# Performance work log

Measured on AMD Instinct MI355X. Metric: run time of the kernel, lower is better.

Reference implementation:

```python
import jax, jax.numpy as jnp
import numpy as np

DIM, CDIM, CSIZE = 512, 128, 8192
EPS = 1e-6


def setup_inputs() -> dict:
    key = jax.random.key(0)
    k = jax.random.split(key, 5)
    x = jax.random.normal(k[0], (4, 4096, DIM), jnp.float32)
    codebook = jax.random.normal(k[1], (CSIZE, CDIM), jnp.float32) * CDIM ** -0.5
    W1 = jax.random.normal(k[2], (CDIM, DIM), jnp.float32) * CDIM ** -0.5
    b1 = jnp.zeros((DIM,), jnp.float32)
    W2 = jax.random.normal(k[3], (DIM, DIM), jnp.float32) * DIM ** -0.5
    b2 = jnp.zeros((DIM,), jnp.float32)
    return dict(x=x, codebook=codebook, W1=W1, b1=b1, W2=W2, b2=b2)


def _code_transform(cb, W1, b1, W2, b2):
    # linear then residual(SELU -> linear):  h + Linear(SELU(h))
    h = cb @ W1 + b1                      # [C, dim]
    return h + jax.nn.selu(h) @ W2 + b2


def _rotate_to(src, tgt):
    # Householder-based rotation trick; only src (=x) carries gradient.
    ns = jnp.linalg.norm(src, axis=-1, keepdims=True)
    nt = jnp.linalg.norm(tgt, axis=-1, keepdims=True)
    u = jax.lax.stop_gradient(src / jnp.maximum(ns, EPS))
    q = jax.lax.stop_gradient(tgt / jnp.maximum(nt, EPS))
    w = u + q
    w = jax.lax.stop_gradient(w / jnp.maximum(jnp.linalg.norm(w, axis=-1, keepdims=True), EPS))
    rot = (src
           - 2.0 * jnp.sum(src * w, -1, keepdims=True) * w
           + 2.0 * jnp.sum(src * u, -1, keepdims=True) * q)
    return rot * jax.lax.stop_gradient(nt / jnp.maximum(ns, EPS))


def reference(x, codebook, W1, b1, W2, b2):
    # implicit codebook through learned transform  [C, dim]
    icb = _code_transform(codebook, W1, b1, W2, b2)
    # nearest-code search (no_grad in original): squared euclidean, argmin
    x_sg = jax.lax.stop_gradient(x)
    icb_sg = jax.lax.stop_gradient(icb)
    d2 = (jnp.sum(x_sg * x_sg, -1, keepdims=True)
          - 2.0 * jnp.einsum('bnd,cd->bnc', x_sg, icb_sg)
          + jnp.sum(icb_sg * icb_sg, -1))          # [B,N,C]
    indices = jnp.argmin(d2, axis=-1)               # [B,N]
    quantized = icb[indices]                        # [B,N,dim]
    commit_loss = (jnp.mean((jax.lax.stop_gradient(x) - quantized) ** 2)
                   + 0.25 * jnp.mean((x - jax.lax.stop_gradient(quantized)) ** 2))
    quantized = _rotate_to(x, quantized)
    return quantized, indices, commit_loss
```

## Files before the change

kernel.cpp:

```cpp
#include <hip/hip_runtime.h>
#include <math.h>

#define DIM   512
#define CDIM  128
#define CSIZE 8192
#define NTOK  16384
#define EPSV  1e-6f
#define NSLICE 8

#define SELU_SCALE 1.0507009873554805f
#define SELU_ALPHA 1.6732632423543772f

typedef __bf16 bf16x8 __attribute__((ext_vector_type(8)));
typedef float  f32x4  __attribute__((ext_vector_type(4)));
typedef unsigned short u16x8 __attribute__((ext_vector_type(8)));

__device__ __forceinline__ float selu_f(float v) {
    return SELU_SCALE * (v > 0.f ? v : SELU_ALPHA * expm1f(v));
}

__device__ __forceinline__ unsigned short b16(float f) {
    unsigned u = __float_as_uint(f);
    u += 0x7FFFu + ((u >> 16) & 1u);
    return (unsigned short)(u >> 16);
}
__device__ __forceinline__ float b2f(unsigned short h) {
    return __uint_as_float(((unsigned)h) << 16);
}

__device__ __forceinline__ unsigned SWZ(unsigned b) {
    return b ^ (((b >> 6) & 14u) << 3);
}

#define GLOAD16(g, l) __builtin_amdgcn_global_load_lds( \
    (const __attribute__((address_space(1))) void*)(g),  \
    (__attribute__((address_space(3))) void*)(l), 16, 0, 0)

__global__ __launch_bounds__(256) void k_init(float* __restrict__ rn2,
                                              float* __restrict__ lossacc) {
    const int i = blockIdx.x * 256 + threadIdx.x;
    if (i < CSIZE) rn2[i] = 0.f;
    if (i < 64)    lossacc[i] = 0.f;
}

__global__ void k_fin(const float* __restrict__ lossacc, float* __restrict__ out_loss) {
    float v = lossacc[threadIdx.x];
#pragma unroll
    for (int o = 1; o < 64; o <<= 1) v += __shfl_xor(v, o);
    if (threadIdx.x == 0)
        out_loss[0] = 1.25f * v / (float)((size_t)NTOK * DIM);
}

__global__ __launch_bounds__(256) void k_split(const float* __restrict__ in,
                                               unsigned short* __restrict__ hi,
                                               unsigned short* __restrict__ lo,
                                               int n4) {
    const int i = blockIdx.x * 256 + threadIdx.x;
    if (i >= n4) return;
    const float4 v = ((const float4*)in)[i];
    const unsigned short h0 = b16(v.x), h1 = b16(v.y), h2 = b16(v.z), h3 = b16(v.w);
    const unsigned short l0 = b16(v.x - b2f(h0));
    const unsigned short l1 = b16(v.y - b2f(h1));
    const unsigned short l2 = b16(v.z - b2f(h2));
    const unsigned short l3 = b16(v.w - b2f(h3));
    ((ushort4*)hi)[i] = make_ushort4(h0, h1, h2, h3);
    ((ushort4*)lo)[i] = make_ushort4(l0, l1, l2, l3);
}

__global__ __launch_bounds__(256) void k_splitT(const float* __restrict__ W,
                                                unsigned short* __restrict__ Thi,
                                                unsigned short* __restrict__ Tlo,
                                                int K, int N) {
    __shared__ float t[32][33];
    const int tx = threadIdx.x & 31, ty = threadIdx.x >> 5;
    const int n0 = blockIdx.x * 32, k0 = blockIdx.y * 32;
#pragma unroll
    for (int i = 0; i < 4; ++i)
        t[ty + i * 8][tx] = W[(size_t)(k0 + ty + i * 8) * N + n0 + tx];
    __syncthreads();
#pragma unroll
    for (int i = 0; i < 4; ++i) {
        const int n = n0 + ty + i * 8, k = k0 + tx;
        const float v = t[tx][ty + i * 8];
        const unsigned short h = b16(v);
        Thi[(size_t)n * K + k] = h;
        Tlo[(size_t)n * K + k] = b16(v - b2f(h));
    }
}

template<int KTOT, bool OUT_SPLIT>
__global__ __launch_bounds__(256) void k_gemm(const float* __restrict__ A,
                                              const unsigned short* __restrict__ BThi,
                                              const unsigned short* __restrict__ BTlo,
                                              const float* __restrict__ bias,
                                              const float* __restrict__ res,
                                              float* __restrict__ outF,
                                              unsigned short* __restrict__ outHi,
                                              unsigned short* __restrict__ outLo,
                                              float* __restrict__ rn2) {
    __shared__ __align__(16) unsigned char smem[24576];
    const int tid = threadIdx.x;
    const int wave = tid >> 6, lane = tid & 63;
    const int l15 = lane & 15, l4 = lane >> 4;
    const int m0 = blockIdx.x * 128, n0 = blockIdx.y * 64;
    const int wm0 = (wave >> 1) * 64, wn0 = (wave & 1) * 32;

    const unsigned LB = SWZ((unsigned)tid * 16u);
    const int soffB = (int)(LB >> 6) * KTOT + (int)((LB >> 4) & 3) * 8;

    const unsigned ra0 = SWZ((unsigned)((wm0 + l15) * 64 + l4 * 16));
    const unsigned rb0 = SWZ((unsigned)((wn0 + l15) * 64 + l4 * 16));

    f32x4 acc[4][2];
#pragma unroll
    for (int a = 0; a < 4; ++a)
#pragma unroll
        for (int b = 0; b < 2; ++b) acc[a][b] = (f32x4)(0.f);

    for (int k0 = 0; k0 < KTOT; k0 += 32) {
        __syncthreads();
        GLOAD16(BThi + (size_t)n0 * KTOT + k0 + soffB, smem + 16384 + wave * 1024);
        GLOAD16(BTlo + (size_t)n0 * KTOT + k0 + soffB, smem + 20480 + wave * 1024);
#pragma unroll
        for (int r = 0; r < 2; ++r) {
            const unsigned g = (unsigned)(tid + r * 256) * 16u;
            const int grow = (int)(g >> 6), gel = (int)((g >> 4) & 3) * 8;
            const float4 v0 = *(const float4*)(A + (size_t)(m0 + grow) * KTOT + k0 + gel);
            const float4 v1 = *(const float4*)(A + (size_t)(m0 + grow) * KTOT + k0 + gel + 4);
            float s[8] = {v0.x, v0.y, v0.z, v0.w, v1.x, v1.y, v1.z, v1.w};
            u16x8 hv, lv;
#pragma unroll
            for (int j = 0; j < 8; ++j) {
                const float sv = OUT_SPLIT ? selu_f(s[j]) : s[j];
                const unsigned short hb = b16(sv);
                hv[j] = hb;
                lv[j] = b16(sv - b2f(hb));
            }
            const unsigned d = SWZ(g);
            *(u16x8*)(smem + d) = hv;
            *(u16x8*)(smem + 8192 + d) = lv;
        }
        __syncthreads();

        bf16x8 bh[2], bl[2];
#pragma unroll
        for (int ni = 0; ni < 2; ++ni) {
            bh[ni] = *(const bf16x8*)(smem + 16384 + rb0 + ni * 1024);
            bl[ni] = *(const bf16x8*)(smem + 20480 + rb0 + ni * 1024);
        }
#pragma unroll
        for (int mi = 0; mi < 4; ++mi) {
            const bf16x8 ah = *(const bf16x8*)(smem + ra0 + mi * 1024);
            const bf16x8 al = *(const bf16x8*)(smem + 8192 + ra0 + mi * 1024);
#pragma unroll
            for (int ni = 0; ni < 2; ++ni) {
                acc[mi][ni] = __builtin_amdgcn_mfma_f32_16x16x32_bf16(ah, bh[ni], acc[mi][ni], 0, 0, 0);
                acc[mi][ni] = __builtin_amdgcn_mfma_f32_16x16x32_bf16(ah, bl[ni], acc[mi][ni], 0, 0, 0);
                acc[mi][ni] = __builtin_amdgcn_mfma_f32_16x16x32_bf16(al, bh[ni], acc[mi][ni], 0, 0, 0);
            }
        }
    }
#pragma unroll
    for (int mi = 0; mi < 4; ++mi)
#pragma unroll
        for (int rr = 0; rr < 4; ++rr) {
            const int m = m0 + wm0 + mi * 16 + l4 * 4 + rr;
            float s2 = 0.f;
#pragma unroll
            for (int ni = 0; ni < 2; ++ni) {
                const int n = n0 + wn0 + ni * 16 + l15;
                float v = acc[mi][ni][rr] + bias[n];
                if constexpr (OUT_SPLIT) {
                    v += res[(size_t)m * DIM + n];
                    const unsigned short hb = b16(v);
                    outHi[(size_t)m * DIM + n] = hb;
                    outLo[(size_t)m * DIM + n] = b16(v - b2f(hb));
                    s2 = fmaf(v, v, s2);
                } else {
                    outF[(size_t)m * DIM + n] = v;
                }
            }
            if constexpr (OUT_SPLIT) {
#pragma unroll
                for (int o = 1; o < 16; o <<= 1) s2 += __shfl_xor(s2, o);
                if (l15 == 0) atomicAdd(&rn2[m], s2);
            }
        }
}

__global__ __launch_bounds__(512, 2) void k_dist(const unsigned short* __restrict__ xh,
                                                 const unsigned short* __restrict__ xl,
                                                 const unsigned short* __restrict__ ch,
                                                 const unsigned short* __restrict__ cl,
                                                 const float* __restrict__ rn2,
                                                 float* __restrict__ pval,
                                                 int*   __restrict__ pidx) {
    __shared__ __align__(16) unsigned char smem[131072];
    const int tid  = threadIdx.x;
    const int wave = tid >> 6, lane = tid & 63;
    const int l15 = lane & 15, l4 = lane >> 4;
    const int m0   = blockIdx.x * 256;
    const int wm0  = (wave >> 1) * 64;
    const int wn0  = (wave & 1) * 128;

    const unsigned LS = SWZ((unsigned)tid * 16u);
    const int soff0 = (int)(LS >> 6) * DIM + (int)((LS >> 4) & 3) * 8;

    const unsigned ra0 = SWZ((unsigned)((wm0 + l15) * 64 + l4 * 16));
    const unsigned rb0 = SWZ((unsigned)((wn0 + l15) * 64 + l4 * 16));

    const unsigned short* xhb = xh + (size_t)m0 * DIM;
    const unsigned short* xlb = xl + (size_t)m0 * DIM;
    const int cbase = blockIdx.y * (CSIZE / NSLICE);

    constexpr int NT   = (CSIZE / NSLICE) / 256;
    constexpr int TOTI = NT * (DIM / 32);

    auto stage = [&](int iter, unsigned bufbase) {
        const int nt2 = iter >> 4;
        const int k0n = (iter & 15) * 32;
        const int sA  = soff0 + k0n;
        const size_t cb0 = (size_t)(cbase + nt2 * 256) * DIM;
#pragma unroll
        for (int r = 0; r < 2; ++r) {
            GLOAD16(xhb + sA + r * 128 * DIM,      smem + bufbase + 0     + r * 8192 + wave * 1024);
            GLOAD16(xlb + sA + r * 128 * DIM,      smem + bufbase + 16384 + r * 8192 + wave * 1024);
            GLOAD16(ch + cb0 + sA + r * 128 * DIM, smem + bufbase + 32768 + r * 8192 + wave * 1024);
            GLOAD16(cl + cb0 + sA + r * 128 * DIM, smem + bufbase + 49152 + r * 8192 + wave * 1024);
        }
    };

    float bestv[4][4];
    int   besti[4][4];
#pragma unroll
    for (int a = 0; a < 4; ++a)
#pragma unroll
        for (int b = 0; b < 4; ++b) { bestv[a][b] = 3.0e38f; besti[a][b] = 0; }

    stage(0, 0u);
    __syncthreads();
    unsigned cur = 0;

    for (int nt = 0; nt < NT; ++nt) {
        f32x4 acc[4][8];
#pragma unroll
        for (int a = 0; a < 4; ++a)
#pragma unroll
            for (int b = 0; b < 8; ++b) acc[a][b] = (f32x4)(0.f);

        for (int ks = 0; ks < 16; ++ks) {
            const int iter = nt * 16 + ks;
            if (iter + 1 < TOTI) stage(iter + 1, (cur ^ 1u) * 65536u);

            const unsigned char* base = smem + cur * 65536u;
            bf16x8 ah[4], al[4];
#pragma unroll
            for (int mi = 0; mi < 4; ++mi) {
                ah[mi] = *(const bf16x8*)(base + ra0 + mi * 1024);
                al[mi] = *(const bf16x8*)(base + 16384 + ra0 + mi * 1024);
            }
#pragma unroll
            for (int ni = 0; ni < 8; ++ni) {
                const bf16x8 bh = *(const bf16x8*)(base + 32768 + rb0 + ni * 1024);
                const bf16x8 bl = *(const bf16x8*)(base + 49152 + rb0 + ni * 1024);
#pragma unroll
                for (int mi = 0; mi < 4; ++mi) {
                    acc[mi][ni] = __builtin_amdgcn_mfma_f32_16x16x32_bf16(ah[mi], bh, acc[mi][ni], 0, 0, 0);
                    acc[mi][ni] = __builtin_amdgcn_mfma_f32_16x16x32_bf16(ah[mi], bl, acc[mi][ni], 0, 0, 0);
                    acc[mi][ni] = __builtin_amdgcn_mfma_f32_16x16x32_bf16(al[mi], bh, acc[mi][ni], 0, 0, 0);
                }
            }
            __syncthreads();
            cur ^= 1u;
        }

        const int n0 = cbase + nt * 256;
#pragma unroll
        for (int ni = 0; ni < 8; ++ni) {
            const int n = n0 + wn0 + ni * 16 + l15;
            const float r = rn2[n];
#pragma unroll
            for (int mi = 0; mi < 4; ++mi)
#pragma unroll
                for (int rr = 0; rr < 4; ++rr) {
                    const float v = fmaf(-2.f, acc[mi][ni][rr], r);
                    if (v < bestv[mi][rr]) { bestv[mi][rr] = v; besti[mi][rr] = n; }
                }
        }
    }

    __syncthreads();
    float* vbuf = (float*)smem;
    int*   ibuf = (int*)(smem + 2048);
#pragma unroll
    for (int mi = 0; mi < 4; ++mi)
#pragma unroll
        for (int rr = 0; rr < 4; ++rr) {
            float v = bestv[mi][rr];
            int   id = besti[mi][rr];
#pragma unroll
            for (int o = 1; o < 16; o <<= 1) {
                const float ov = __shfl_xor(v, o);
                const int   oid = __shfl_xor(id, o);
                if (ov < v || (ov == v && oid < id)) { v = ov; id = oid; }
            }
            if (l15 == 0) {
                const int ml = wm0 + mi * 16 + l4 * 4 + rr;
                vbuf[(wave & 1) * 256 + ml] = v;
                ibuf[(wave & 1) * 256 + ml] = id;
            }
        }
    __syncthreads();
    if (tid < 256) {
        const int ml = tid;
        float v0 = vbuf[ml], v1 = vbuf[256 + ml];
        int   i0 = ibuf[ml], i1 = ibuf[256 + ml];
        if (v1 < v0 || (v1 == v0 && i1 < i0)) { v0 = v1; i0 = i1; }
        pval[(size_t)blockIdx.y * NTOK + m0 + ml] = v0;
        pidx[(size_t)blockIdx.y * NTOK + m0 + ml] = i0;
    }
}

__global__ __launch_bounds__(256) void k_epi(const float* __restrict__ x,
                                             const unsigned short* __restrict__ chi,
                                             const unsigned short* __restrict__ clo,
                                             const float* __restrict__ pval,
                                             const int*   __restrict__ pidx,
                                             float* __restrict__ out_q,
                                             float* __restrict__ out_idx,
                                             float* __restrict__ lossacc) {
    const int wave = threadIdx.x >> 6, lane = threadIdx.x & 63;
    const int t = blockIdx.x * 4 + wave;

    float v = 3.0e38f; int id = 0;
    if (lane < NSLICE) {
        v  = pval[(size_t)lane * NTOK + t];
        id = pidx[(size_t)lane * NTOK + t];
    }
#pragma unroll
    for (int o = 1; o < 16; o <<= 1) {
        const float ov = __shfl_xor(v, o);
        const int   oid = __shfl_xor(id, o);
        if (ov < v || (ov == v && oid < id)) { v = ov; id = oid; }
    }
    id = __shfl(id, 0);

    const float4* xp = (const float4*)(x + (size_t)t * DIM);
    const float4 xv0 = xp[lane * 2];
    const float4 xv1 = xp[lane * 2 + 1];
    const u16x8 hv = *(const u16x8*)(chi + (size_t)id * DIM + lane * 8);
    const u16x8 lv = *(const u16x8*)(clo + (size_t)id * DIM + lane * 8);
    float q[8], xs[8] = {xv0.x, xv0.y, xv0.z, xv0.w, xv1.x, xv1.y, xv1.z, xv1.w};
#pragma unroll
    for (int j = 0; j < 8; ++j) q[j] = b2f(hv[j]) + b2f(lv[j]);

    float p0 = 0.f, p1 = 0.f, p2 = 0.f;
#pragma unroll
    for (int j = 0; j < 8; ++j) {
        p0 = fmaf(xs[j], xs[j], p0);
        p1 = fmaf(q[j], q[j], p1);
        p2 = fmaf(xs[j], q[j], p2);
    }
#pragma unroll
    for (int o = 1; o < 64; o <<= 1) {
        p0 += __shfl_xor(p0, o);
        p1 += __shfl_xor(p1, o);
        p2 += __shfl_xor(p2, o);
    }
    const float sx2 = p0, sq2 = p1, sxq = p2;

    const float ns  = sqrtf(sx2);
    const float nt  = sqrtf(sq2);
    const float nsc = fmaxf(ns, EPSV);
    const float ntc = fmaxf(nt, EPSV);
    const float xu  = sx2 / nsc;
    const float xqh = sxq / ntc;
    const float xw0 = xu + xqh;
    const float w0n2 = sx2 / (nsc * nsc) + 2.f * sxq / (nsc * ntc) + sq2 / (ntc * ntc);
    const float w0nc = fmaxf(sqrtf(w0n2), EPSV);
    const float coefW = 2.f * xw0 / (w0nc * w0nc);
    const float coefQ = 2.f * xu / ntc;
    const float scale = nt / nsc;
    const float cx = scale * (1.f - coefW / nsc);
    const float cq = scale * (coefQ - coefW / ntc);

    float4 ov0, ov1;
    ov0.x = cx * xs[0] + cq * q[0];  ov0.y = cx * xs[1] + cq * q[1];
    ov0.z = cx * xs[2] + cq * q[2];  ov0.w = cx * xs[3] + cq * q[3];
    ov1.x = cx * xs[4] + cq * q[4];  ov1.y = cx * xs[5] + cq * q[5];
    ov1.z = cx * xs[6] + cq * q[6];  ov1.w = cx * xs[7] + cq * q[7];
    ((float4*)(out_q + (size_t)t * DIM))[lane * 2]     = ov0;
    ((float4*)(out_q + (size_t)t * DIM))[lane * 2 + 1] = ov1;

    __shared__ float sew[4];
    if (lane == 0) {
        out_idx[t] = (float)id;
        sew[wave] = sx2 - 2.f * sxq + sq2;
    }
    __syncthreads();
    if (threadIdx.x == 0) {
        const float se = sew[0] + sew[1] + sew[2] + sew[3];
        atomicAdd(lossacc + (blockIdx.x & 63), se);
    }
}

extern "C" void kernel_launch(void* const* d_in, const int* in_sizes, int n_in,
                              void* d_out, int out_size, void* d_ws, size_t ws_size,
                              hipStream_t stream) {
    const float* x  = (const float*)d_in[0];
    const float* cb = (const float*)d_in[1];
    const float* W1 = (const float*)d_in[2];
    const float* b1 = (const float*)d_in[3];
    const float* W2 = (const float*)d_in[4];
    const float* b2 = (const float*)d_in[5];

    char* ws = (char*)d_ws;
    float* h = (float*)ws;
    unsigned short* chi = (unsigned short*)(h + (size_t)CSIZE * DIM);
    unsigned short* clo = chi + (size_t)CSIZE * DIM;
    unsigned short* W1Thi = clo + (size_t)CSIZE * DIM;
    unsigned short* W1Tlo = W1Thi + (size_t)DIM * CDIM;
    unsigned short* W2Thi = W1Tlo + (size_t)DIM * CDIM;
    unsigned short* W2Tlo = W2Thi + (size_t)DIM * DIM;
    float* rn2  = (float*)(W2Tlo + (size_t)DIM * DIM);
    float* pval = rn2 + CSIZE;
    int*   pidx = (int*)(pval + (size_t)NSLICE * NTOK);
    float* lossacc = (float*)(pidx + (size_t)NSLICE * NTOK);

    unsigned short* xhi = (unsigned short*)d_out;
    unsigned short* xlo = xhi + (size_t)NTOK * DIM;

    float* out_q    = (float*)d_out;
    float* out_idx  = out_q + (size_t)NTOK * DIM;
    float* out_loss = out_idx + NTOK;

    k_init<<<(CSIZE + 255) / 256, 256, 0, stream>>>(rn2, lossacc);
    k_split<<<(NTOK * DIM / 4) / 256, 256, 0, stream>>>(x, xhi, xlo, NTOK * DIM / 4);
    k_splitT<<<dim3(DIM / 32, CDIM / 32), 256, 0, stream>>>(W1, W1Thi, W1Tlo, CDIM, DIM);
    k_splitT<<<dim3(DIM / 32, DIM / 32), 256, 0, stream>>>(W2, W2Thi, W2Tlo, DIM, DIM);
    k_gemm<CDIM, false><<<dim3(CSIZE / 128, DIM / 64), 256, 0, stream>>>(
        cb, W1Thi, W1Tlo, b1, nullptr, h, nullptr, nullptr, nullptr);
    k_gemm<DIM, true><<<dim3(CSIZE / 128, DIM / 64), 256, 0, stream>>>(
        h, W2Thi, W2Tlo, b2, h, nullptr, chi, clo, rn2);
    k_dist<<<dim3(NTOK / 256, NSLICE), 512, 0, stream>>>(xhi, xlo, chi, clo, rn2, pval, pidx);
    k_epi<<<NTOK / 4, 256, 0, stream>>>(x, chi, clo, pval, pidx, out_q, out_idx, lossacc);
    k_fin<<<1, 64, 0, stream>>>(lossacc, out_loss);
}
```

Measured before the change: 485.5 us.

## Load distance-kernel A operands directly into registers and shrink blocks to 128 tokens

The distance kernel now stages only the codebook tile in shared memory. The token hi/lo fragments are loaded straight from global memory into double-buffered registers, and blocks shrink to 256 threads and 128 tokens with half the LDS. The in-block cross-wave argmin reduction through shared memory is dropped. Each wave writes its own partial result, so the epilogue now reduces 16 slices instead of 8. MFMA sections get raised wave priority. This removes LDS traffic and barriers for A, at the cost of uncoalesced per-lane global loads for A and doubled codebook re-reads across blocks.

```diff
diff --git a/kernel.cpp b/kernel.cpp
--- a/kernel.cpp
+++ b/kernel.cpp
@@ -7,6 +7,7 @@
 #define NTOK  16384
 #define EPSV  1e-6f
 #define NSLICE 8
+#define NSLICE2 16
 
 #define SELU_SCALE 1.0507009873554805f
 #define SELU_ALPHA 1.6732632423543772f
@@ -188,45 +189,49 @@
         }
 }
 
-__global__ __launch_bounds__(512, 2) void k_dist(const unsigned short* __restrict__ xh,
+__global__ __launch_bounds__(256, 2) void k_dist(const unsigned short* __restrict__ xh,
                                                  const unsigned short* __restrict__ xl,
                                                  const unsigned short* __restrict__ ch,
                                                  const unsigned short* __restrict__ cl,
                                                  const float* __restrict__ rn2,
                                                  float* __restrict__ pval,
                                                  int*   __restrict__ pidx) {
-    __shared__ __align__(16) unsigned char smem[131072];
+    __shared__ __align__(16) unsigned char smem[65536];
     const int tid  = threadIdx.x;
     const int wave = tid >> 6, lane = tid & 63;
     const int l15 = lane & 15, l4 = lane >> 4;
-    const int m0   = blockIdx.x * 256;
+    const int m0   = blockIdx.x * 128;
     const int wm0  = (wave >> 1) * 64;
     const int wn0  = (wave & 1) * 128;
 
     const unsigned LS = SWZ((unsigned)tid * 16u);
     const int soff0 = (int)(LS >> 6) * DIM + (int)((LS >> 4) & 3) * 8;
 
-    const unsigned ra0 = SWZ((unsigned)((wm0 + l15) * 64 + l4 * 16));
     const unsigned rb0 = SWZ((unsigned)((wn0 + l15) * 64 + l4 * 16));
 
-    const unsigned short* xhb = xh + (size_t)m0 * DIM;
-    const unsigned short* xlb = xl + (size_t)m0 * DIM;
+    const unsigned short* xhb = xh + (size_t)(m0 + wm0 + l15) * DIM + l4 * 8;
+    const unsigned short* xlb = xl + (size_t)(m0 + wm0 + l15) * DIM + l4 * 8;
+
     const int cbase = blockIdx.y * (CSIZE / NSLICE);
-
     constexpr int NT   = (CSIZE / NSLICE) / 256;
-    constexpr int TOTI = NT * (DIM / 32);
-
-    auto stage = [&](int iter, unsigned bufbase) {
-        const int nt2 = iter >> 4;
-        const int k0n = (iter & 15) * 32;
-        const int sA  = soff0 + k0n;
-        const size_t cb0 = (size_t)(cbase + nt2 * 256) * DIM;
-#pragma unroll
-        for (int r = 0; r < 2; ++r) {
-            GLOAD16(xhb + sA + r * 128 * DIM,      smem + bufbase + 0     + r * 8192 + wave * 1024);
-            GLOAD16(xlb + sA + r * 128 * DIM,      smem + bufbase + 16384 + r * 8192 + wave * 1024);
-            GLOAD16(ch + cb0 + sA + r * 128 * DIM, smem + bufbase + 32768 + r * 8192 + wave * 1024);
-            GLOAD16(cl + cb0 + sA + r * 128 * DIM, smem + bufbase + 49152 + r * 8192 + wave * 1024);
+    constexpr int TOTI = NT * 16;
+
+    auto stageB = [&](int it, unsigned bufbase) {
+        const size_t cb0 = (size_t)(cbase + (it >> 4) * 256) * DIM + (it & 15) * 32 + soff0;
+#pragma unroll
+        for (int r = 0; r < 4; ++r) {
+            GLOAD16(ch + cb0 + r * 64 * DIM, smem + bufbase + 0     + r * 4096 + wave * 1024);
+            GLOAD16(cl + cb0 + r * 64 * DIM, smem + bufbase + 16384 + r * 4096 + wave * 1024);
+        }
+    };
+
+    bf16x8 aH[2][4], aL[2][4];
+    auto loadA = [&](int it, int par) {
+        const int k0 = (it & 15) * 32;
+#pragma unroll
+        for (int f = 0; f < 4; ++f) {
+            aH[par][f] = *(const bf16x8*)(xhb + (size_t)f * 16 * DIM + k0);
+            aL[par][f] = *(const bf16x8*)(xlb + (size_t)f * 16 * DIM + k0);
         }
     };
 
@@ -237,7 +242,8 @@
 #pragma unroll
         for (int b = 0; b < 4; ++b) { bestv[a][b] = 3.0e38f; besti[a][b] = 0; }
 
-    stage(0, 0u);
+    stageB(0, 0u);
+    loadA(0, 0);
     __syncthreads();
     unsigned cur = 0;
 
@@ -248,28 +254,27 @@
 #pragma unroll
             for (int b = 0; b < 8; ++b) acc[a][b] = (f32x4)(0.f);
 
+#pragma unroll
         for (int ks = 0; ks < 16; ++ks) {
-            const int iter = nt * 16 + ks;
-            if (iter + 1 < TOTI) stage(iter + 1, (cur ^ 1u) * 65536u);
-
-            const unsigned char* base = smem + cur * 65536u;
-            bf16x8 ah[4], al[4];
-#pragma unroll
-            for (int mi = 0; mi < 4; ++mi) {
-                ah[mi] = *(const bf16x8*)(base + ra0 + mi * 1024);
-                al[mi] = *(const bf16x8*)(base + 16384 + ra0 + mi * 1024);
-            }
+            const int it = nt * 16 + ks;
+            if (it + 1 < TOTI) {
+                stageB(it + 1, (cur ^ 1u) * 32768u);
+                loadA(it + 1, (ks + 1) & 1);
+            }
+            const unsigned char* base = smem + cur * 32768u;
+            __builtin_amdgcn_s_setprio(1);
 #pragma unroll
             for (int ni = 0; ni < 8; ++ni) {
-                const bf16x8 bh = *(const bf16x8*)(base + 32768 + rb0 + ni * 1024);
-                const bf16x8 bl = *(const bf16x8*)(base + 49152 + rb0 + ni * 1024);
+                const bf16x8 bh = *(const bf16x8*)(base + rb0 + ni * 1024);
+                const bf16x8 bl = *(const bf16x8*)(base + 16384 + rb0 + ni * 1024);
 #pragma unroll
                 for (int mi = 0; mi < 4; ++mi) {
-                    acc[mi][ni] = __builtin_amdgcn_mfma_f32_16x16x32_bf16(ah[mi], bh, acc[mi][ni], 0, 0, 0);
-                    acc[mi][ni] = __builtin_amdgcn_mfma_f32_16x16x32_bf16(ah[mi], bl, acc[mi][ni], 0, 0, 0);
-                    acc[mi][ni] = __builtin_amdgcn_mfma_f32_16x16x32_bf16(al[mi], bh, acc[mi][ni], 0, 0, 0);
+                    acc[mi][ni] = __builtin_amdgcn_mfma_f32_16x16x32_bf16(aH[ks & 1][mi], bh, acc[mi][ni], 0, 0, 0);
+                    acc[mi][ni] = __builtin_amdgcn_mfma_f32_16x16x32_bf16(aH[ks & 1][mi], bl, acc[mi][ni], 0, 0, 0);
+                    acc[mi][ni] = __builtin_amdgcn_mfma_f32_16x16x32_bf16(aL[ks & 1][mi], bh, acc[mi][ni], 0, 0, 0);
                 }
             }
+            __builtin_amdgcn_s_setprio(0);
             __syncthreads();
             cur ^= 1u;
         }
@@ -289,9 +294,7 @@
         }
     }
 
-    __syncthreads();
-    float* vbuf = (float*)smem;
-    int*   ibuf = (int*)(smem + 2048);
+    const int slice = blockIdx.y * 2 + (wave & 1);
 #pragma unroll
     for (int mi = 0; mi < 4; ++mi)
 #pragma unroll
@@ -305,20 +308,11 @@
                 if (ov < v || (ov == v && oid < id)) { v = ov; id = oid; }
             }
             if (l15 == 0) {
-                const int ml = wm0 + mi * 16 + l4 * 4 + rr;
-                vbuf[(wave & 1) * 256 + ml] = v;
-                ibuf[(wave & 1) * 256 + ml] = id;
-            }
-        }
-    __syncthreads();
-    if (tid < 256) {
-        const int ml = tid;
-        float v0 = vbuf[ml], v1 = vbuf[256 + ml];
-        int   i0 = ibuf[ml], i1 = ibuf[256 + ml];
-        if (v1 < v0 || (v1 == v0 && i1 < i0)) { v0 = v1; i0 = i1; }
-        pval[(size_t)blockIdx.y * NTOK + m0 + ml] = v0;
-        pidx[(size_t)blockIdx.y * NTOK + m0 + ml] = i0;
-    }
+                const int m = m0 + wm0 + mi * 16 + l4 * 4 + rr;
+                pval[(size_t)slice * NTOK + m] = v;
+                pidx[(size_t)slice * NTOK + m] = id;
+            }
+        }
 }
 
 __global__ __launch_bounds__(256) void k_epi(const float* __restrict__ x,
@@ -333,7 +327,7 @@
     const int t = blockIdx.x * 4 + wave;
 
     float v = 3.0e38f; int id = 0;
-    if (lane < NSLICE) {
+    if (lane < NSLICE2) {
         v  = pval[(size_t)lane * NTOK + t];
         id = pidx[(size_t)lane * NTOK + t];
     }
@@ -424,8 +418,8 @@
     unsigned short* W2Tlo = W2Thi + (size_t)DIM * DIM;
     float* rn2  = (float*)(W2Tlo + (size_t)DIM * DIM);
     float* pval = rn2 + CSIZE;
-    int*   pidx = (int*)(pval + (size_t)NSLICE * NTOK);
-    float* lossacc = (float*)(pidx + (size_t)NSLICE * NTOK);
+    int*   pidx = (int*)(pval + (size_t)NSLICE2 * NTOK);
+    float* lossacc = (float*)(pidx + (size_t)NSLICE2 * NTOK);
 
     unsigned short* xhi = (unsigned short*)d_out;
     unsigned short* xlo = xhi + (size_t)NTOK * DIM;
@@ -442,7 +436,7 @@
         cb, W1Thi, W1Tlo, b1, nullptr, h, nullptr, nullptr, nullptr);
     k_gemm<DIM, true><<<dim3(CSIZE / 128, DIM / 64), 256, 0, stream>>>(
         h, W2Thi, W2Tlo, b2, h, nullptr, chi, clo, rn2);
-    k_dist<<<dim3(NTOK / 256, NSLICE), 512, 0, stream>>>(xhi, xlo, chi, clo, rn2, pval, pidx);
+    k_dist<<<dim3(NTOK / 128, NSLICE), 256, 0, stream>>>(xhi, xlo, chi, clo, rn2, pval, pidx);
     k_epi<<<NTOK / 4, 256, 0, stream>>>(x, chi, clo, pval, pidx, out_q, out_idx, lossacc);
     k_fin<<<1, 64, 0, stream>>>(lossacc, out_loss);
 }
```

New measurement: 1.008 ms. 2.08x slower.
